# Performance work log

Hardware: AMD Instinct MI355X
Metric: run time of the kernel (lower is better)

The kernel has to match this reference:

```python
import jax, jax.numpy as jnp
import numpy as np

H = 16
HD = 128
ROPE_BASE = 10000.0

def _rope_cos_sin(T, dtype):
    inv_freq = 1.0 / (ROPE_BASE ** (jnp.arange(0, HD, 2, dtype=jnp.float32) / HD))  # [HD/2]
    pos = jnp.arange(T, dtype=jnp.float32)
    freqs = pos[:, None] * inv_freq[None, :]  # [T, HD/2]
    return jnp.cos(freqs).astype(dtype), jnp.sin(freqs).astype(dtype)

def _apply_rotary(x, cos, sin):
    # x: [B,H,T,HD]; cos/sin: [T,HD/2]
    x1, x2 = x[..., : HD // 2], x[..., HD // 2 :]
    c = cos[None, None, :, :]
    s = sin[None, None, :, :]
    return jnp.concatenate([x1 * c - x2 * s, x1 * s + x2 * c], axis=-1)

def setup_inputs() -> dict:
    key = jax.random.key(0)
    ks = jax.random.split(key, 5)
    B, T, D = 2, 2048, 2048
    x = jax.random.normal(ks[0], (B, T, D), dtype=jnp.float32)
    Wqkv = jax.random.normal(ks[1], (3 * D, D), dtype=jnp.float32) * (D ** -0.5)
    bqkv = jax.random.normal(ks[2], (3 * D,), dtype=jnp.float32) * 0.02
    Wo = jax.random.normal(ks[3], (D, D), dtype=jnp.float32) * (D ** -0.5)
    bo = jax.random.normal(ks[4], (D,), dtype=jnp.float32) * 0.02
    # causal mask: True = masked (future positions)
    mask = jnp.triu(jnp.ones((T, T), dtype=bool), k=1)[None, None, :, :]
    return {"x": x, "Wqkv": Wqkv, "bqkv": bqkv, "Wo": Wo, "bo": bo, "mask": mask}

def reference(x, Wqkv, bqkv, Wo, bo, mask):
    B, T, D = x.shape
    qkv = x @ Wqkv.T + bqkv  # [B,T,3D]
    q, k, v = jnp.split(qkv, 3, axis=-1)
    def to_heads(t):
        return t.reshape(B, T, H, HD).transpose(0, 2, 1, 3)  # [B,H,T,HD]
    q, k, v = to_heads(q), to_heads(k), to_heads(v)
    cos, sin = _rope_cos_sin(T, x.dtype)
    q = _apply_rotary(q, cos, sin)
    k = _apply_rotary(k, cos, sin)
    scale = HD ** 0.5
    attn = jnp.einsum('bhqd,bhkd->bhqk', q, k) / scale
    neg = -jnp.finfo(x.dtype).max
    attn = jnp.where(mask, neg, attn)
    w = jax.nn.softmax(attn, axis=-1)
    out = jnp.einsum('bhqk,bhkd->bhqd', w, v)  # [B,H,T,HD]
    out = out.transpose(0, 2, 1, 3).reshape(B, T, H * HD)
    return out @ Wo.T + bo
```

## Files before the change

kernel.cpp:

```cpp
#include <hip/hip_runtime.h>
#include <hip/hip_bf16.h>
#include <cstdint>

typedef __bf16 bf16;
typedef __bf16 bf16x8 __attribute__((ext_vector_type(8)));
typedef float  f32x4  __attribute__((ext_vector_type(4)));

#define B_   2
#define T_   2048
#define D_   2048
#define H_   16
#define HD_  128

typedef __attribute__((address_space(3))) void       lds_void;
typedef __attribute__((address_space(1))) const void gbl_void;
__device__ __forceinline__ void glds16(const bf16* g, bf16* l) {
    __builtin_amdgcn_global_load_lds((gbl_void*)g, (lds_void*)l, 16, 0, 0);
}

__device__ __forceinline__ ushort4 cvt4(const float4 v) {
    union { bf16 h[4]; ushort4 u; } pk;
    pk.h[0] = (bf16)v.x; pk.h[1] = (bf16)v.y;
    pk.h[2] = (bf16)v.z; pk.h[3] = (bf16)v.w;
    return pk.u;
}

__global__ __launch_bounds__(256) void convert_xw_kernel(
    const float* __restrict__ x, const float* __restrict__ wqkv,
    bf16* __restrict__ xb, bf16* __restrict__ wqkvb)
{
    const int NX = (B_ * T_ * D_) / 4;
    const int NT = NX + (3 * D_ * D_) / 4;
    for (int g = blockIdx.x * blockDim.x + threadIdx.x; g < NT;
         g += gridDim.x * blockDim.x) {
        if (g < NX) ((ushort4*)xb)[g]      = cvt4(((const float4*)x)[g]);
        else        ((ushort4*)wqkvb)[g-NX] = cvt4(((const float4*)wqkv)[g-NX]);
    }
}

__global__ __launch_bounds__(256) void convert_wo_kernel(
    const float* __restrict__ wo, bf16* __restrict__ wob)
{
    const int N = (D_ * D_) / 4;
    for (int g = blockIdx.x * blockDim.x + threadIdx.x; g < N;
         g += gridDim.x * blockDim.x)
        ((ushort4*)wob)[g] = cvt4(((const float4*)wo)[g]);
}

__device__ __forceinline__ void gemm_core_glds(
    const bf16* __restrict__ A, const bf16* __restrict__ W, int K,
    int bm, int bn, int tid, f32x4 (&acc)[4][4],
    bf16* lds_a, bf16* lds_b)
{
    const int lane = tid & 63, quad = lane >> 4, lcol = lane & 15;
    const int wave = tid >> 6;
    const int wm = (wave >> 1) * 64, wn2 = (wave & 1) * 32;
    const int sw = lcol & 7;
    const int sr = tid >> 3, pc = tid & 7;
    const int sc = (pc ^ (sr & 7)) * 8;
    const bf16* abase = A + (size_t)(bm * 128 + sr) * K + sc;
    const bf16* bbase = W + (size_t)(bn * 128 + sr) * K + sc;
    bf16* la = lds_a + sr * 64 + pc * 8;
    bf16* lb = lds_b + sr * 64 + pc * 8;

    for (int k0 = 0; k0 < K; k0 += 64) {
        __syncthreads();
#pragma unroll
        for (int p = 0; p < 4; p++) {
            glds16(abase + k0 + (size_t)32 * p * K, la + 2048 * p);
            glds16(bbase + k0 + (size_t)32 * p * K, lb + 2048 * p);
        }
        __syncthreads();
#pragma unroll
        for (int kk = 0; kk < 2; kk++) {
            bf16x8 af[4], bfr[4];
#pragma unroll
            for (int i = 0; i < 4; i++)
                af[i] = *(const bf16x8*)&lds_a[(wm + i * 16 + lcol) * 64 +
                                               (((kk * 4 + quad) ^ sw) * 8)];
#pragma unroll
            for (int j = 0; j < 4; j++) {
                const int row = wn2 + (j & 1) * 16 + (j >> 1) * 64 + lcol;
                bfr[j] = *(const bf16x8*)&lds_b[row * 64 +
                                                (((kk * 4 + quad) ^ sw) * 8)];
            }
#pragma unroll
            for (int i = 0; i < 4; i++)
#pragma unroll
                for (int j = 0; j < 4; j++)
                    acc[i][j] = __builtin_amdgcn_mfma_f32_16x16x32_bf16(af[i], bfr[j], acc[i][j], 0, 0, 0);
        }
    }
}

__global__ __launch_bounds__(256) void qkv_gemm_kernel(
    const bf16* __restrict__ xb, const bf16* __restrict__ wqkvb,
    const float* __restrict__ bias,
    bf16* __restrict__ qh, bf16* __restrict__ kh, bf16* __restrict__ vT)
{
    __shared__ bf16 lds_a[128 * 64];
    __shared__ bf16 lds_b[128 * 64];
    const int tid = threadIdx.x;
    const int bm = blockIdx.y, bn = blockIdx.x;
    const int lane = tid & 63, quad = lane >> 4, lcol = lane & 15;
    const int wave = tid >> 6;
    const int wm = (wave >> 1) * 64, wn2 = (wave & 1) * 32;

    f32x4 acc[4][4];
    const f32x4 z = {0.f, 0.f, 0.f, 0.f};
#pragma unroll
    for (int i = 0; i < 4; i++)
#pragma unroll
        for (int j = 0; j < 4; j++) acc[i][j] = z;

    gemm_core_glds(xb, wqkvb, D_, bm, bn, tid, acc, lds_a, lds_b);

    const int n0 = bn * 128;
    const int part = bn / 16;
    const int h = bn & 15;
    const int mb0 = bm * 128 + wm;

    if (part < 2) {
        bf16* dst = (part == 0) ? qh : kh;
#pragma unroll
        for (int i = 0; i < 4; i++) {
#pragma unroll
            for (int jp = 0; jp < 2; jp++) {
                const int d1 = wn2 + jp * 16 + lcol;
                const float invf = __expf(-0.14391156831212787f * (float)d1);
                const float b1 = bias[n0 + d1];
                const float b2 = bias[n0 + d1 + 64];
#pragma unroll
                for (int r = 0; r < 4; r++) {
                    const int m = mb0 + i * 16 + quad * 4 + r;
                    const int bb = m >> 11, t = m & (T_ - 1);
                    const float x1 = acc[i][jp][r] + b1;
                    const float x2 = acc[i][jp + 2][r] + b2;
                    float s, c;
                    __sincosf((float)t * invf, &s, &c);
                    const size_t rowo = ((size_t)(bb * H_ + h) * T_ + t) * HD_;
                    dst[rowo + d1]      = (bf16)(x1 * c - x2 * s);
                    dst[rowo + d1 + 64] = (bf16)(x1 * s + x2 * c);
                }
            }
        }
    } else {
        const int bb = mb0 >> 11, t64 = mb0 & (T_ - 1);
        const int bh = bb * H_ + h;
#pragma unroll
        for (int j = 0; j < 4; j++) {
            const int d = wn2 + (j & 1) * 16 + (j >> 1) * 64 + lcol;
            const float bv = bias[n0 + d];
            bf16* vdst = &vT[((size_t)bh * HD_ + d) * T_ + t64];
#pragma unroll
            for (int r = 0; r < 4; r++) {
                union { bf16 hh[4]; ushort4 u; } pk;
#pragma unroll
                for (int i = 0; i < 4; i++) pk.hh[i] = (bf16)(acc[i][j][r] + bv);
                *(ushort4*)&vdst[(quad * 4 + r) * 4] = pk.u;
            }
        }
    }
}

__global__ __launch_bounds__(256) void attn_kernel(
    const bf16* __restrict__ qh, const bf16* __restrict__ kh,
    const bf16* __restrict__ vT, bf16* __restrict__ ctx)
{
    __shared__ bf16 lds_k[2][64 * 128];
    __shared__ bf16 lds_v[2][128 * 64];
    __shared__ bf16 lds_p[64 * 64];
    const int tid = threadIdx.x;
    const int id = blockIdx.x;
    const int bh = id & 31;
    const int q5 = (id >> 5) & 15;
    const int qt = (id >> 9) ? (31 - q5) : q5;
    const int q0 = qt * 64;
    const int lane = tid & 63, quad = lane >> 4, lcol = lane & 15;
    const int wave = tid >> 6;
    const int wq0 = wave * 16;
    const float scale2 = 0.08838834764831845f * 1.4426950408889634f;

    const bf16* kbase = kh + (size_t)bh * T_ * HD_;
    const bf16* vbase = vT + (size_t)bh * HD_ * T_;

    const int ksrow = tid >> 4;
    const bf16* kstage = kbase + (size_t)ksrow * HD_ + (((tid & 15) ^ ksrow) << 3);
    const int vsd = tid >> 3;
    const bf16* vstage = vbase + (size_t)vsd * T_ + (((tid & 7) ^ (vsd & 7)) << 3);

    bf16x8 qf[4];
#pragma unroll
    for (int kk = 0; kk < 4; kk++)
        qf[kk] = *(const bf16x8*)&qh[((size_t)bh * T_ + q0 + wq0 + lcol) * HD_ +
                                     kk * 32 + quad * 8];

    f32x4 o[8];
    const f32x4 z = {0.f, 0.f, 0.f, 0.f};
#pragma unroll
    for (int jd = 0; jd < 8; jd++) o[jd] = z;
    float l_part[4] = {0.f, 0.f, 0.f, 0.f};

    const int ktmax = qt + 1;
#pragma unroll
    for (int p = 0; p < 4; p++) {
        glds16(kstage + (size_t)16 * p * HD_, &lds_k[0][tid * 8 + p * 2048]);
        glds16(vstage + (size_t)32 * p * T_, &lds_v[0][tid * 8 + p * 2048]);
    }

    for (int kt = 0; kt < ktmax; kt++) {
        __syncthreads();
        if (kt + 1 < ktmax) {
            const bf16* ks = kstage + (size_t)(kt + 1) * 64 * HD_;
            const bf16* vs = vstage + (kt + 1) * 64;
            bf16* lkd = &lds_k[(kt + 1) & 1][tid * 8];
            bf16* lvd = &lds_v[(kt + 1) & 1][tid * 8];
#pragma unroll
            for (int p = 0; p < 4; p++) {
                glds16(ks + (size_t)16 * p * HD_, lkd + p * 2048);
                glds16(vs + (size_t)32 * p * T_, lvd + p * 2048);
            }
        }
        const bf16* lk = lds_k[kt & 1];
        const bf16* lv = lds_v[kt & 1];

        f32x4 s_acc[4];
#pragma unroll
        for (int j = 0; j < 4; j++) s_acc[j] = z;
        __builtin_amdgcn_s_setprio(1);
#pragma unroll
        for (int kk = 0; kk < 4; kk++) {
#pragma unroll
            for (int j = 0; j < 4; j++) {
                const bf16x8 bk = *(const bf16x8*)&lk[(j * 16 + lcol) * 128 +
                                        (((kk * 4 + quad) ^ lcol) << 3)];
                s_acc[j] = __builtin_amdgcn_mfma_f32_16x16x32_bf16(qf[kk], bk, s_acc[j], 0, 0, 0);
            }
        }
        __builtin_amdgcn_s_setprio(0);

        const bool diag = (kt == qt);
#pragma unroll
        for (int r = 0; r < 4; r++) {
            const int prow = wq0 + quad * 4 + r;
            const int qrow = q0 + prow;
            union { bf16 hh[4]; ushort4 u; } pk;
            float lp = 0.f;
#pragma unroll
            for (int j = 0; j < 4; j++) {
                float p = exp2f(fmaf(s_acc[j][r], scale2, -16.0f));
                if (diag) {
                    const int kcol = kt * 64 + j * 16 + lcol;
                    p = (kcol > qrow) ? 0.f : p;
                }
                lp += p;
                pk.hh[j] = (bf16)p;
            }
            l_part[r] += lp;
            *(ushort4*)&lds_p[prow * 64 + ((lcol * 4) ^ ((prow & 7) << 3))] = pk.u;
        }

#pragma unroll
        for (int kk2 = 0; kk2 < 2; kk2++) {
            const int prow = wq0 + lcol;
            const bf16x8 pf = *(const bf16x8*)&lds_p[prow * 64 +
                                  ((kk2 * 32 + quad * 8) ^ ((lcol & 7) << 3))];
            bf16x8 vf[8];
#pragma unroll
            for (int jd = 0; jd < 8; jd++) {
                const int d = jd * 16 + lcol;
                vf[jd] = *(const bf16x8*)&lv[d * 64 +
                              (((kk2 * 4 + quad) ^ (lcol & 7)) << 3)];
            }
            __builtin_amdgcn_s_setprio(1);
#pragma unroll
            for (int jd = 0; jd < 8; jd++)
                o[jd] = __builtin_amdgcn_mfma_f32_16x16x32_bf16(pf, vf[jd], o[jd], 0, 0, 0);
            __builtin_amdgcn_s_setprio(0);
        }
    }

    float inv_l[4];
#pragma unroll
    for (int r = 0; r < 4; r++) {
        float rs = l_part[r];
#pragma unroll
        for (int off = 1; off < 16; off <<= 1)
            rs += __shfl_xor(rs, off);
        inv_l[r] = 1.0f / rs;
    }
    const int b = bh >> 4, h = bh & 15;
#pragma unroll
    for (int r = 0; r < 4; r++) {
        const int t = q0 + wq0 + quad * 4 + r;
#pragma unroll
        for (int jd = 0; jd < 8; jd++)
            ctx[((size_t)(b * T_ + t)) * D_ + h * HD_ + jd * 16 + lcol] =
                (bf16)(o[jd][r] * inv_l[r]);
    }
}

__global__ __launch_bounds__(256) void proj_gemm_kernel(
    const bf16* __restrict__ ctx, const bf16* __restrict__ wob,
    const float* __restrict__ bias, float* __restrict__ out)
{
    __shared__ bf16 lds_a[128 * 64];
    __shared__ bf16 lds_b[128 * 64];
    const int tid = threadIdx.x;
    const int bm = blockIdx.y, bn = blockIdx.x;
    const int lane = tid & 63, quad = lane >> 4, lcol = lane & 15;
    const int wave = tid >> 6;
    const int wm = (wave >> 1) * 64, wn2 = (wave & 1) * 32;

    f32x4 acc[4][4];
    const f32x4 z = {0.f, 0.f, 0.f, 0.f};
#pragma unroll
    for (int i = 0; i < 4; i++)
#pragma unroll
        for (int j = 0; j < 4; j++) acc[i][j] = z;

    gemm_core_glds(ctx, wob, D_, bm, bn, tid, acc, lds_a, lds_b);

    const int n0 = bn * 128;
#pragma unroll
    for (int i = 0; i < 4; i++) {
#pragma unroll
        for (int j = 0; j < 4; j++) {
            const int n = n0 + wn2 + (j & 1) * 16 + (j >> 1) * 64 + lcol;
            const float bv = bias[n];
#pragma unroll
            for (int r = 0; r < 4; r++) {
                const int m = bm * 128 + wm + i * 16 + quad * 4 + r;
                out[(size_t)m * D_ + n] = acc[i][j][r] + bv;
            }
        }
    }
}

extern "C" void kernel_launch(void* const* d_in, const int* in_sizes, int n_in,
                              void* d_out, int out_size, void* d_ws, size_t ws_size,
                              hipStream_t stream)
{
    const float* x    = (const float*)d_in[0];
    const float* Wqkv = (const float*)d_in[1];
    const float* bqkv = (const float*)d_in[2];
    const float* Wo   = (const float*)d_in[3];
    const float* bo   = (const float*)d_in[4];
    float* out = (float*)d_out;

    const size_t HT = (size_t)B_ * H_ * T_ * HD_;
    bf16* xb   = (bf16*)d_ws;
    bf16* qh   = xb + HT;
    bf16* kh   = qh + HT;
    bf16* vT   = kh + HT;
    bf16* ctx  = xb;
    bf16* wob  = qh;
    bf16* wqkvb = (bf16*)d_out;

    convert_xw_kernel<<<2560, 256, 0, stream>>>(x, Wqkv, xb, wqkvb);
    qkv_gemm_kernel<<<dim3(48, 32), 256, 0, stream>>>(xb, wqkvb, bqkv, qh, kh, vT);
    attn_kernel<<<1024, 256, 0, stream>>>(qh, kh, vT, ctx);
    convert_wo_kernel<<<1024, 256, 0, stream>>>(Wo, wob);
    proj_gemm_kernel<<<dim3(16, 32), 256, 0, stream>>>(ctx, wob, bo, out);
}
```

Before: 353.5 us.

## Enlarge attention query tile to 128 rows with two sub-tiles per wave

```diff
diff --git a/kernel.cpp b/kernel.cpp
--- a/kernel.cpp
+++ b/kernel.cpp
@@ -163,22 +163,22 @@
     }
 }
 
-__global__ __launch_bounds__(256) void attn_kernel(
+__global__ __launch_bounds__(256, 2) void attn_kernel(
     const bf16* __restrict__ qh, const bf16* __restrict__ kh,
     const bf16* __restrict__ vT, bf16* __restrict__ ctx)
 {
     __shared__ bf16 lds_k[2][64 * 128];
     __shared__ bf16 lds_v[2][128 * 64];
-    __shared__ bf16 lds_p[64 * 64];
+    __shared__ bf16 lds_p[128 * 64];
     const int tid = threadIdx.x;
     const int id = blockIdx.x;
     const int bh = id & 31;
-    const int q5 = (id >> 5) & 15;
-    const int qt = (id >> 9) ? (31 - q5) : q5;
-    const int q0 = qt * 64;
+    const int q4 = (id >> 5) & 7;
+    const int qt = (id >> 8) ? (15 - q4) : q4;
+    const int q0 = qt * 128;
     const int lane = tid & 63, quad = lane >> 4, lcol = lane & 15;
     const int wave = tid >> 6;
-    const int wq0 = wave * 16;
+    const int wq0 = wave * 32;
     const float scale2 = 0.08838834764831845f * 1.4426950408889634f;
 
     const bf16* kbase = kh + (size_t)bh * T_ * HD_;
@@ -189,19 +189,30 @@
     const int vsd = tid >> 3;
     const bf16* vstage = vbase + (size_t)vsd * T_ + (((tid & 7) ^ (vsd & 7)) << 3);
 
-    bf16x8 qf[4];
-#pragma unroll
-    for (int kk = 0; kk < 4; kk++)
-        qf[kk] = *(const bf16x8*)&qh[((size_t)bh * T_ + q0 + wq0 + lcol) * HD_ +
-                                     kk * 32 + quad * 8];
-
-    f32x4 o[8];
+    bf16x8 qf[2][4];
+#pragma unroll
+    for (int i = 0; i < 2; i++)
+#pragma unroll
+        for (int kk = 0; kk < 4; kk++)
+            qf[i][kk] = *(const bf16x8*)&qh[((size_t)bh * T_ + q0 + wq0 + i * 16 + lcol) * HD_ +
+                                            kk * 32 + quad * 8];
+
+    f32x4 o[2][8];
     const f32x4 z = {0.f, 0.f, 0.f, 0.f};
 #pragma unroll
-    for (int jd = 0; jd < 8; jd++) o[jd] = z;
-    float l_part[4] = {0.f, 0.f, 0.f, 0.f};
-
-    const int ktmax = qt + 1;
+    for (int i = 0; i < 2; i++)
+#pragma unroll
+        for (int jd = 0; jd < 8; jd++) o[i][jd] = z;
+    float l_part[2][4];
+#pragma unroll
+    for (int i = 0; i < 2; i++)
+#pragma unroll
+        for (int r = 0; r < 4; r++) l_part[i][r] = 0.f;
+
+    const int wrow_min = q0 + wq0;
+    const int wrow_max = wrow_min + 31;
+
+    const int ktmax = 2 * qt + 2;
 #pragma unroll
     for (int p = 0; p < 4; p++) {
         glds16(kstage + (size_t)16 * p * HD_, &lds_k[0][tid * 8 + p * 2048]);
@@ -221,12 +232,16 @@
                 glds16(vs + (size_t)32 * p * T_, lvd + p * 2048);
             }
         }
+        if (kt * 64 > wrow_max) continue;
+        const bool needmask = (kt * 64 + 63 > wrow_min);
         const bf16* lk = lds_k[kt & 1];
         const bf16* lv = lds_v[kt & 1];
 
-        f32x4 s_acc[4];
-#pragma unroll
-        for (int j = 0; j < 4; j++) s_acc[j] = z;
+        f32x4 s_acc[2][4];
+#pragma unroll
+        for (int i = 0; i < 2; i++)
+#pragma unroll
+            for (int j = 0; j < 4; j++) s_acc[i][j] = z;
         __builtin_amdgcn_s_setprio(1);
 #pragma unroll
         for (int kk = 0; kk < 4; kk++) {
@@ -234,38 +249,45 @@
             for (int j = 0; j < 4; j++) {
                 const bf16x8 bk = *(const bf16x8*)&lk[(j * 16 + lcol) * 128 +
                                         (((kk * 4 + quad) ^ lcol) << 3)];
-                s_acc[j] = __builtin_amdgcn_mfma_f32_16x16x32_bf16(qf[kk], bk, s_acc[j], 0, 0, 0);
+#pragma unroll
+                for (int i = 0; i < 2; i++)
+                    s_acc[i][j] = __builtin_amdgcn_mfma_f32_16x16x32_bf16(qf[i][kk], bk, s_acc[i][j], 0, 0, 0);
             }
         }
         __builtin_amdgcn_s_setprio(0);
 
-        const bool diag = (kt == qt);
-#pragma unroll
-        for (int r = 0; r < 4; r++) {
-            const int prow = wq0 + quad * 4 + r;
-            const int qrow = q0 + prow;
-            union { bf16 hh[4]; ushort4 u; } pk;
-            float lp = 0.f;
-#pragma unroll
-            for (int j = 0; j < 4; j++) {
-                float p = exp2f(fmaf(s_acc[j][r], scale2, -16.0f));
-                if (diag) {
-                    const int kcol = kt * 64 + j * 16 + lcol;
-                    p = (kcol > qrow) ? 0.f : p;
+#pragma unroll
+        for (int i = 0; i < 2; i++) {
+#pragma unroll
+            for (int r = 0; r < 4; r++) {
+                const int prow = wq0 + i * 16 + quad * 4 + r;
+                const int qrow = q0 + prow;
+                union { bf16 hh[4]; ushort4 u; } pk;
+                float lp = 0.f;
+#pragma unroll
+                for (int j = 0; j < 4; j++) {
+                    float p = exp2f(fmaf(s_acc[i][j][r], scale2, -16.0f));
+                    if (needmask) {
+                        const int kcol = kt * 64 + j * 16 + lcol;
+                        p = (kcol > qrow) ? 0.f : p;
+                    }
+                    lp += p;
+                    pk.hh[j] = (bf16)p;
                 }
-                lp += p;
-                pk.hh[j] = (bf16)p;
-            }
-            l_part[r] += lp;
-            *(ushort4*)&lds_p[prow * 64 + ((lcol * 4) ^ ((prow & 7) << 3))] = pk.u;
+                l_part[i][r] += lp;
+                *(ushort4*)&lds_p[prow * 64 + ((lcol * 4) ^ ((prow & 7) << 3))] = pk.u;
+            }
         }
 
 #pragma unroll
         for (int kk2 = 0; kk2 < 2; kk2++) {
-            const int prow = wq0 + lcol;
-            const bf16x8 pf = *(const bf16x8*)&lds_p[prow * 64 +
-                                  ((kk2 * 32 + quad * 8) ^ ((lcol & 7) << 3))];
-            bf16x8 vf[8];
+            bf16x8 pf[2], vf[8];
+#pragma unroll
+            for (int i = 0; i < 2; i++) {
+                const int prow = wq0 + i * 16 + lcol;
+                pf[i] = *(const bf16x8*)&lds_p[prow * 64 +
+                            ((kk2 * 32 + quad * 8) ^ ((lcol & 7) << 3))];
+            }
 #pragma unroll
             for (int jd = 0; jd < 8; jd++) {
                 const int d = jd * 16 + lcol;
@@ -274,29 +296,36 @@
             }
             __builtin_amdgcn_s_setprio(1);
 #pragma unroll
+            for (int i = 0; i < 2; i++)
+#pragma unroll
+                for (int jd = 0; jd < 8; jd++)
+                    o[i][jd] = __builtin_amdgcn_mfma_f32_16x16x32_bf16(pf[i], vf[jd], o[i][jd], 0, 0, 0);
+            __builtin_amdgcn_s_setprio(0);
+        }
+    }
+
+    float inv_l[2][4];
+#pragma unroll
+    for (int i = 0; i < 2; i++)
+#pragma unroll
+        for (int r = 0; r < 4; r++) {
+            float rs = l_part[i][r];
+#pragma unroll
+            for (int off = 1; off < 16; off <<= 1)
+                rs += __shfl_xor(rs, off);
+            inv_l[i][r] = 1.0f / rs;
+        }
+    const int b = bh >> 4, h = bh & 15;
+#pragma unroll
+    for (int i = 0; i < 2; i++) {
+#pragma unroll
+        for (int r = 0; r < 4; r++) {
+            const int t = q0 + wq0 + i * 16 + quad * 4 + r;
+#pragma unroll
             for (int jd = 0; jd < 8; jd++)
-                o[jd] = __builtin_amdgcn_mfma_f32_16x16x32_bf16(pf, vf[jd], o[jd], 0, 0, 0);
-            __builtin_amdgcn_s_setprio(0);
-        }
-    }
-
-    float inv_l[4];
-#pragma unroll
-    for (int r = 0; r < 4; r++) {
-        float rs = l_part[r];
-#pragma unroll
-        for (int off = 1; off < 16; off <<= 1)
-            rs += __shfl_xor(rs, off);
-        inv_l[r] = 1.0f / rs;
-    }
-    const int b = bh >> 4, h = bh & 15;
-#pragma unroll
-    for (int r = 0; r < 4; r++) {
-        const int t = q0 + wq0 + quad * 4 + r;
-#pragma unroll
-        for (int jd = 0; jd < 8; jd++)
-            ctx[((size_t)(b * T_ + t)) * D_ + h * HD_ + jd * 16 + lcol] =
-                (bf16)(o[jd][r] * inv_l[r]);
+                ctx[((size_t)(b * T_ + t)) * D_ + h * HD_ + jd * 16 + lcol] =
+                    (bf16)(o[i][jd][r] * inv_l[i][r]);
+        }
     }
 }
 
@@ -359,7 +388,7 @@
 
     convert_xw_kernel<<<2560, 256, 0, stream>>>(x, Wqkv, xb, wqkvb);
     qkv_gemm_kernel<<<dim3(48, 32), 256, 0, stream>>>(xb, wqkvb, bqkv, qh, kh, vT);
-    attn_kernel<<<1024, 256, 0, stream>>>(qh, kh, vT, ctx);
+    attn_kernel<<<512, 256, 0, stream>>>(qh, kh, vT, ctx);
     convert_wo_kernel<<<1024, 256, 0, stream>>>(Wo, wob);
     proj_gemm_kernel<<<dim3(16, 32), 256, 0, stream>>>(ctx, wob, bo, out);
 }
```

Result: slower. 374.2 us (+5.8%).
